# Kernel optimization log

Measured on AMD Instinct MI355X. Metric: run time of the kernel, lower is better.

## Reference

```python
import jax, jax.numpy as jnp
import numpy as np

N_NODES = 20000
N_EDGES = 40000
H = 64          # n_hidden
F_ATOM = 62     # n_atom_features (< H, triggers zero-pad path)
F_BOND = 6      # n_bond_features
B = 512         # number of graphs in batch
T = 2           # message passing steps


def setup_inputs() -> dict:
    key = jax.random.key(0)
    ks = jax.random.split(key, 20)
    s = 0.05  # small init scale to avoid selu/tanh saturation
    inp = {
        'node_features': jax.random.normal(ks[0], (N_NODES, F_ATOM), jnp.float32),
        'edge_features': jax.random.normal(ks[1], (N_EDGES, F_BOND), jnp.float32),
        'edge_domain': jax.random.randint(ks[2], (N_EDGES,), 0, N_NODES, jnp.int32),
        'edge_range': jax.random.randint(ks[3], (N_EDGES,), 0, N_NODES, jnp.int32),
        'graph_id': jnp.sort(jax.random.randint(ks[4], (N_NODES,), 0, B, jnp.int32)),
        # EdgeNetwork params (weights stored [in, out], i.e. torch W.T)
        'Wm': jax.random.normal(ks[5], (F_BOND, H), jnp.float32) * s,
        'bm': jnp.zeros((H,), jnp.float32),
        'Ew': jax.random.normal(ks[6], (H, H * H), jnp.float32) * s,  # E.weight used as mm(mlp, E.weight): [H, H*H]
        # update2 linears (T=2)
        'Wu0': jax.random.normal(ks[7], (H, H), jnp.float32) * s,
        'bu0': jnp.zeros((H,), jnp.float32),
        'Wu1': jax.random.normal(ks[8], (H, H), jnp.float32) * s,
        'bu1': jnp.zeros((H,), jnp.float32),
        # atom_embed
        'Wae': jax.random.normal(ks[9], (H, H), jnp.float32) * s,
        'bae': jnp.zeros((H,), jnp.float32),
        # AggregateReadout.R
        'WR': jax.random.normal(ks[10], (H, H), jnp.float32) * s,
        'bR': jnp.zeros((H,), jnp.float32),
        # mlp + out head
        'Wmlp': jax.random.normal(ks[11], (H, H), jnp.float32) * s,
        'bmlp': jnp.zeros((H,), jnp.float32),
        'Wout': jax.random.normal(ks[12], (H, 1), jnp.float32) * s,
        'bout': jnp.zeros((1,), jnp.float32),
    }
    return inp


def reference(node_features, edge_features, edge_domain, edge_range, graph_id,
              Wm, bm, Ew, Wu0, bu0, Wu1, bu1, Wae, bae, WR, bR,
              Wmlp, bmlp, Wout, bout):
    # pad node features up to n_hidden (original zero-pads when narrower)
    h = jnp.pad(node_features, ((0, 0), (0, H - F_ATOM)))  # [N, H]

    # EdgeNetwork: edge-conditioned per-edge HxH weight matrix.
    # Edge features are constant across T, so A is identical each step;
    # compute once (original recomputes the same values every iteration).
    mlp_features = jax.nn.relu(edge_features @ Wm + bm)      # [E, H]
    A = (mlp_features @ Ew).reshape(-1, H, H)                # [E, H, H]

    for Wu, bu in ((Wu0, bu0), (Wu1, bu1)):
        hj = h[edge_range]                                   # gather [E, H]
        edge_message = jnp.einsum('eij,ej->ei', A, hj)       # bmm [E, H]
        message = jax.ops.segment_sum(edge_message, edge_domain,
                                      num_segments=N_NODES)  # scatter-add [N, H]
        h = jax.nn.selu(message @ Wu + bu + h)

    atom_embedding = h @ Wae + bae                           # [N, H]
    # AggregateReadout
    atom_activation = jax.nn.selu(atom_embedding @ WR + bR)  # [N, H]
    graph_sum = jax.ops.segment_sum(atom_activation, graph_id, num_segments=B)
    graph_embedding = jnp.tanh(graph_sum)                    # [B, H]

    mlp_out = jax.nn.relu(graph_embedding @ Wmlp + bmlp)     # [B, H]
    out = mlp_out @ Wout + bout                              # [B, 1]
    return out.reshape(-1, 1)
```

## Files before the change

kernel.cpp:

```cpp
#include <hip/hip_runtime.h>
#include <math.h>

#define NN 20000
#define NE 40000
#define H 64
#define F_ATOM 62
#define F_BOND 6
#define NB 512

typedef _Float16 f16x8 __attribute__((ext_vector_type(8)));
typedef float f32x16 __attribute__((ext_vector_type(16)));

__device__ __forceinline__ float selu_f(float x) {
    const float scale = 1.0507009873554805f;
    const float alpha = 1.6732632423543772f;
    return scale * (x > 0.0f ? x : alpha * (__expf(x) - 1.0f));
}

__device__ __forceinline__ f16x8 splat8h(_Float16 x) {
    union { _Float16 h[2]; unsigned u; } p;
    p.h[0] = x; p.h[1] = x;
    union { unsigned u[4]; f16x8 v; } r;
    r.u[0] = p.u; r.u[1] = p.u; r.u[2] = p.u; r.u[3] = p.u;
    return r.v;
}

__global__ void prep_kernel(const float* __restrict__ nf, const float* __restrict__ ef,
                            const float* __restrict__ Wm, const float* __restrict__ bm,
                            const float* __restrict__ Ew,
                            _Float16* __restrict__ h_h,
                            unsigned* __restrict__ mlp2, _Float16* __restrict__ ewb,
                            float* __restrict__ msg, float* __restrict__ gsum) {
    const int bid = blockIdx.x;
    const int t = threadIdx.x;
    if (bid < 625) {
        __shared__ float st[64][65];
        const int el = t & 63;
        const int ig = t >> 6;
        const int e = bid * 64 + el;
        const float* efe = ef + e * F_BOND;
        const float e0 = efe[0], e1 = efe[1], e2 = efe[2];
        const float e3 = efe[3], e4 = efe[4], e5 = efe[5];
#pragma unroll
        for (int p = 0; p < 16; ++p) {
            const int i = ig * 16 + p;
            float s = bm[i];
            s = fmaf(e0, Wm[0 * H + i], s);
            s = fmaf(e1, Wm[1 * H + i], s);
            s = fmaf(e2, Wm[2 * H + i], s);
            s = fmaf(e3, Wm[3 * H + i], s);
            s = fmaf(e4, Wm[4 * H + i], s);
            s = fmaf(e5, Wm[5 * H + i], s);
            st[i][el] = fmaxf(s, 0.0f);
        }
        __syncthreads();
        const int p = t >> 3;
        const int ch = t & 7;
#pragma unroll
        for (int j = 0; j < 8; ++j) {
            const int e_l = ch * 8 + j;
            union { unsigned u; _Float16 hh[2]; } pk;
            pk.hh[0] = (_Float16)st[2 * p][e_l];
            pk.hh[1] = (_Float16)st[2 * p + 1][e_l];
            mlp2[(size_t)p * NE + bid * 64 + e_l] = pk.u;
        }
    } else if (bid < 5625) {
        int idx = (bid - 625) * 256 + t;
        int n = idx >> 6, c = idx & 63;
        h_h[idx] = (_Float16)((c < F_ATOM) ? nf[n * F_ATOM + c] : 0.0f);
    } else if (bid < 5753) {
        int tid = (bid - 5625) * 256 + t;
        int l = tid & 63;
        int nt = (tid >> 6) & 1;
        int c = tid >> 7;
        int kk = c >> 2;
        int jbase = (c & 3) * 16 + (l >> 5) * 8;
        int i = nt * 32 + (l & 31);
        const float* src = Ew + kk * 4096 + i * 64 + jbase;
        _Float16* dst = ewb + tid * 8;
#pragma unroll
        for (int u = 0; u < 8; ++u) dst[u] = (_Float16)src[u];
    } else if (bid < 7003) {
        int idx = (bid - 5753) * 256 + t;
        reinterpret_cast<float4*>(msg)[idx] = make_float4(0.f, 0.f, 0.f, 0.f);
    } else {
        int idx = (bid - 7003) * 256 + t;
        reinterpret_cast<float4*>(gsum)[idx] = make_float4(0.f, 0.f, 0.f, 0.f);
    }
}

__global__ __launch_bounds__(128, 4) void edge_message_mfma(
    const _Float16* __restrict__ h_h, const unsigned* __restrict__ mlp2,
    const int* __restrict__ ed, const int* __restrict__ er,
    const _Float16* __restrict__ ewb, float* __restrict__ msg)
{
    __shared__ char sm[32768];
    __shared__ int edom_s[64];

    const int t = threadIdx.x;
    const int lane = t & 63;
    const int kg = t >> 6;
    const int l31 = lane & 31;
    const int hf = lane >> 5;
    const int kh = blockIdx.x & 1;
    const int eb = (blockIdx.x >> 1) * 64;
    const int kbase = kh * 32 + kg * 16;

    if (t < 64) edom_s[t] = ed[eb + t];

    const int eA = eb + l31;
    const int eB = eA + 32;
    const int gA = er[eA], gB = er[eB];

    f16x8 hjA[4], hjB[4];
#pragma unroll
    for (int cq = 0; cq < 4; ++cq) {
        hjA[cq] = *reinterpret_cast<const f16x8*>(h_h + gA * 64 + cq * 16 + hf * 8);
        hjB[cq] = *reinterpret_cast<const f16x8*>(h_h + gB * 64 + cq * 16 + hf * 8);
    }

    unsigned mvA[8], mvB[8];
#pragma unroll
    for (int pp = 0; pp < 8; ++pp) {
        mvA[pp] = mlp2[(size_t)((kbase >> 1) + pp) * NE + eA];
        mvB[pp] = mlp2[(size_t)((kbase >> 1) + pp) * NE + eB];
    }

    asm volatile("s_waitcnt vmcnt(0)" ::: "memory");

    char* wbase = sm + kg * 16384;
    auto stage = [&](int s) {
        const char* gs = reinterpret_cast<const char*>(ewb) +
                         ((size_t)(kbase + s) << 13) + lane * 16;
        char* lb = wbase + (s & 1) * 8192 + lane * 16;
#pragma unroll
        for (int r = 0; r < 8; ++r) {
            __builtin_amdgcn_global_load_lds(
                (const __attribute__((address_space(1))) void*)(gs + r * 1024),
                (__attribute__((address_space(3))) void*)(lb + r * 1024),
                16, 0, 0);
        }
    };

    f32x16 a00, a01, a10, a11;
#pragma unroll
    for (int i = 0; i < 16; ++i) { a00[i] = 0.f; a01[i] = 0.f; a10[i] = 0.f; a11[i] = 0.f; }

    stage(0);

#pragma unroll
    for (int s = 0; s < 16; ++s) {
        asm volatile("s_waitcnt vmcnt(0)" ::: "memory");
        if (s < 15) stage(s + 1);
        const char* buf = wbase + (s & 1) * 8192;
        union { unsigned u; _Float16 hh[2]; } ua, ub;
        ua.u = mvA[s >> 1]; ub.u = mvB[s >> 1];
        f16x8 sA = splat8h(ua.hh[s & 1]);
        f16x8 sB = splat8h(ub.hh[s & 1]);
        __builtin_amdgcn_s_setprio(1);
#pragma unroll
        for (int cq = 0; cq < 4; ++cq) {
            f16x8 b0 = *reinterpret_cast<const f16x8*>(buf + (cq * 2 + 0) * 1024 + lane * 16);
            f16x8 b1 = *reinterpret_cast<const f16x8*>(buf + (cq * 2 + 1) * 1024 + lane * 16);
            f16x8 aA = sA * hjA[cq];
            f16x8 aB = sB * hjB[cq];
            a00 = __builtin_amdgcn_mfma_f32_32x32x16_f16(aA, b0, a00, 0, 0, 0);
            a01 = __builtin_amdgcn_mfma_f32_32x32x16_f16(aA, b1, a01, 0, 0, 0);
            a10 = __builtin_amdgcn_mfma_f32_32x32x16_f16(aB, b0, a10, 0, 0, 0);
            a11 = __builtin_amdgcn_mfma_f32_32x32x16_f16(aB, b1, a11, 0, 0, 0);
        }
        __builtin_amdgcn_s_setprio(0);
    }

    float* X = reinterpret_cast<float*>(sm);
    __syncthreads();
    if (kg == 1) {
#pragma unroll
        for (int r = 0; r < 16; ++r) {
            const int m = (r & 3) + 8 * (r >> 2) + 4 * hf;
            X[m * 64 + l31]             = a00[r];
            X[m * 64 + 32 + l31]        = a01[r];
            X[(32 + m) * 64 + l31]      = a10[r];
            X[(32 + m) * 64 + 32 + l31] = a11[r];
        }
    }
    __syncthreads();
    if (kg == 0) {
#pragma unroll
        for (int r = 0; r < 16; ++r) {
            const int m = (r & 3) + 8 * (r >> 2) + 4 * hf;
            const int domA = edom_s[m];
            const int domB = edom_s[32 + m];
            atomicAdd(&msg[domA * 64 + l31],      a00[r] + X[m * 64 + l31]);
            atomicAdd(&msg[domA * 64 + 32 + l31], a01[r] + X[m * 64 + 32 + l31]);
            atomicAdd(&msg[domB * 64 + l31],      a10[r] + X[(32 + m) * 64 + l31]);
            atomicAdd(&msg[domB * 64 + 32 + l31], a11[r] + X[(32 + m) * 64 + 32 + l31]);
        }
    }
}

__global__ __launch_bounds__(256) void node_update_kernel(
    float* __restrict__ msg, const float* __restrict__ Wu,
    const float* __restrict__ bu, _Float16* __restrict__ h_h) {
    __shared__ float ms[32][65];
    const int t = threadIdx.x;
    const int nb = blockIdx.x * 32;
#pragma unroll
    for (int r = 0; r < 2; ++r) {
        int idx = r * 256 + t;
        int n = idx >> 4, c4 = (idx & 15) * 4;
        float4* src = reinterpret_cast<float4*>(msg + (size_t)(nb + n) * 64 + c4);
        float4 v = *src;
        *src = make_float4(0.f, 0.f, 0.f, 0.f);
        ms[n][c4 + 0] = v.x; ms[n][c4 + 1] = v.y;
        ms[n][c4 + 2] = v.z; ms[n][c4 + 3] = v.w;
    }
    __syncthreads();
    const int i = t & 63;
    const int n0 = (t >> 6) * 8;
    float acc[8];
#pragma unroll
    for (int j = 0; j < 8; ++j) acc[j] = bu[i];
#pragma unroll 8
    for (int k = 0; k < 64; ++k) {
        float w = Wu[k * 64 + i];
#pragma unroll
        for (int j = 0; j < 8; ++j) acc[j] = fmaf(ms[n0 + j][k], w, acc[j]);
    }
#pragma unroll
    for (int j = 0; j < 8; ++j) {
        int o = (nb + n0 + j) * 64 + i;
        h_h[o] = (_Float16)selu_f(acc[j] + (float)h_h[o]);
    }
}

__global__ __launch_bounds__(256) void upd2_embed_readout(
    const float* __restrict__ msg, const float* __restrict__ Wu,
    const float* __restrict__ bu, const _Float16* __restrict__ h_h,
    const float* __restrict__ Wae, const float* __restrict__ bae,
    const float* __restrict__ WR, const float* __restrict__ bR,
    const int* __restrict__ gid, float* __restrict__ gsum) {
    __shared__ float ms[32][65];
    __shared__ float hn[32][65];
    __shared__ float ae[32][65];
    const int t = threadIdx.x;
    const int nb = blockIdx.x * 32;
#pragma unroll
    for (int r = 0; r < 2; ++r) {
        int idx = r * 256 + t;
        int n = idx >> 4, c4 = (idx & 15) * 4;
        float4 v = *reinterpret_cast<const float4*>(msg + (size_t)(nb + n) * 64 + c4);
        ms[n][c4 + 0] = v.x; ms[n][c4 + 1] = v.y;
        ms[n][c4 + 2] = v.z; ms[n][c4 + 3] = v.w;
    }
    __syncthreads();
    const int i = t & 63;
    const int n0 = (t >> 6) * 8;
    float acc[8];
#pragma unroll
    for (int j = 0; j < 8; ++j) acc[j] = bu[i];
#pragma unroll 8
    for (int k = 0; k < 64; ++k) {
        float w = Wu[k * 64 + i];
#pragma unroll
        for (int j = 0; j < 8; ++j) acc[j] = fmaf(ms[n0 + j][k], w, acc[j]);
    }
#pragma unroll
    for (int j = 0; j < 8; ++j)
        hn[n0 + j][i] = selu_f(acc[j] + (float)h_h[(nb + n0 + j) * 64 + i]);
    __syncthreads();
#pragma unroll
    for (int j = 0; j < 8; ++j) acc[j] = bae[i];
#pragma unroll 8
    for (int k = 0; k < 64; ++k) {
        float w = Wae[k * 64 + i];
#pragma unroll
        for (int j = 0; j < 8; ++j) acc[j] = fmaf(hn[n0 + j][k], w, acc[j]);
    }
#pragma unroll
    for (int j = 0; j < 8; ++j) ae[n0 + j][i] = acc[j];
    __syncthreads();
#pragma unroll
    for (int j = 0; j < 8; ++j) acc[j] = bR[i];
#pragma unroll 8
    for (int k = 0; k < 64; ++k) {
        float w = WR[k * 64 + i];
#pragma unroll
        for (int j = 0; j < 8; ++j) acc[j] = fmaf(ae[n0 + j][k], w, acc[j]);
    }
#pragma unroll
    for (int j = 0; j < 8; ++j)
        atomicAdd(&gsum[gid[nb + n0 + j] * 64 + i], selu_f(acc[j]));
}

__global__ void final_kernel(const float* __restrict__ gsum, const float* __restrict__ Wmlp,
                             const float* __restrict__ bmlp, const float* __restrict__ Wout,
                             const float* __restrict__ bout, float* __restrict__ out) {
    __shared__ float ge[64];
    int g = blockIdx.x, i = threadIdx.x;
    ge[i] = tanhf(gsum[g * H + i]);
    __syncthreads();
    float s = bmlp[i];
#pragma unroll
    for (int k = 0; k < H; ++k) s = fmaf(ge[k], Wmlp[k * H + i], s);
    float mo = fmaxf(s, 0.0f) * Wout[i];
#pragma unroll
    for (int off = 32; off > 0; off >>= 1) mo += __shfl_down(mo, off);
    if (i == 0) out[g] = mo + bout[0];
}

extern "C" void kernel_launch(void* const* d_in, const int* in_sizes, int n_in,
                              void* d_out, int out_size, void* d_ws, size_t ws_size,
                              hipStream_t stream) {
    const float* nf   = (const float*)d_in[0];
    const float* ef   = (const float*)d_in[1];
    const int*   ed   = (const int*)d_in[2];
    const int*   er   = (const int*)d_in[3];
    const int*   gid  = (const int*)d_in[4];
    const float* Wm   = (const float*)d_in[5];
    const float* bm   = (const float*)d_in[6];
    const float* Ew   = (const float*)d_in[7];
    const float* Wu0  = (const float*)d_in[8];
    const float* bu0  = (const float*)d_in[9];
    const float* Wu1  = (const float*)d_in[10];
    const float* bu1  = (const float*)d_in[11];
    const float* Wae  = (const float*)d_in[12];
    const float* bae  = (const float*)d_in[13];
    const float* WR   = (const float*)d_in[14];
    const float* bR   = (const float*)d_in[15];
    const float* Wmlp = (const float*)d_in[16];
    const float* bmlp = (const float*)d_in[17];
    const float* Wout = (const float*)d_in[18];
    const float* bout = (const float*)d_in[19];
    float* out = (float*)d_out;

    float* ws = (float*)d_ws;
    float*    msg  = ws + 1280000;
    float*    gsum = ws + 2560000;
    unsigned* mlp2 = (unsigned*)(ws + 2592768);
    _Float16* h_h  = (_Float16*)(ws + 3872768);
    _Float16* ewb  = (_Float16*)(ws + 4512768);

    prep_kernel<<<7035, 256, 0, stream>>>(nf, ef, Wm, bm, Ew, h_h, mlp2, ewb, msg, gsum);

    edge_message_mfma<<<1250, 128, 0, stream>>>(h_h, mlp2, ed, er, ewb, msg);
    node_update_kernel<<<NN / 32, 256, 0, stream>>>(msg, Wu0, bu0, h_h);
    edge_message_mfma<<<1250, 128, 0, stream>>>(h_h, mlp2, ed, er, ewb, msg);
    upd2_embed_readout<<<NN / 32, 256, 0, stream>>>(msg, Wu1, bu1, h_h,
                                                    Wae, bae, WR, bR, gid, gsum);

    final_kernel<<<NB, 64, 0, stream>>>(gsum, Wmlp, bmlp, Wout, bout, out);
}
```

Before: 137.9 us.

## Keep Ew slices register-resident and stream edge tiles through persistent blocks

The edge message kernel is restructured so that each wave loads a fixed slice of the fp16 Ew weights into registers once. It then loops over five 32-edge tiles, using the weights as the MFMA A operand and the scaled gathered node features as B. This replaces the per-block streaming of weights through LDS with double buffering. Partial sums across the k-split waves are reduced in LDS with shared atomics before global atomics go to msg. The cost is 128 registers of weights per lane, fewer blocks (500 blocks of 512 threads), extra barriers per tile, and LDS atomic contention.

```diff
diff --git a/kernel.cpp b/kernel.cpp
--- a/kernel.cpp
+++ b/kernel.cpp
@@ -29,7 +29,7 @@
                             const float* __restrict__ Wm, const float* __restrict__ bm,
                             const float* __restrict__ Ew,
                             _Float16* __restrict__ h_h,
-                            unsigned* __restrict__ mlp2, _Float16* __restrict__ ewb,
+                            unsigned* __restrict__ mlp2, _Float16* __restrict__ ewA,
                             float* __restrict__ msg, float* __restrict__ gsum) {
     const int bid = blockIdx.x;
     const int t = threadIdx.x;
@@ -70,14 +70,18 @@
         h_h[idx] = (_Float16)((c < F_ATOM) ? nf[n * F_ATOM + c] : 0.0f);
     } else if (bid < 5753) {
         int tid = (bid - 5625) * 256 + t;
-        int l = tid & 63;
-        int nt = (tid >> 6) & 1;
-        int c = tid >> 7;
-        int kk = c >> 2;
-        int jbase = (c & 3) * 16 + (l >> 5) * 8;
-        int i = nt * 32 + (l & 31);
-        const float* src = Ew + kk * 4096 + i * 64 + jbase;
-        _Float16* dst = ewb + tid * 8;
+        const int l = tid & 63;
+        const int f = (tid >> 6) & 31;
+        const int slice = tid >> 11;
+        const int kh = slice >> 3;
+        const int kw = (slice >> 1) & 3;
+        const int ih = slice & 1;
+        const int i = ih * 32 + (l & 31);
+        const int kg = kh * 2048 + kw * 512 + f * 16 + (l >> 5) * 8;
+        const int kk = kg >> 6;
+        const int jb = kg & 63;
+        const float* src = Ew + (size_t)kk * 4096 + i * 64 + jb;
+        _Float16* dst = ewA + (size_t)tid * 8;
 #pragma unroll
         for (int u = 0; u < 8; ++u) dst[u] = (_Float16)src[u];
     } else if (bid < 7003) {
@@ -89,113 +93,85 @@
     }
 }
 
-__global__ __launch_bounds__(128, 4) void edge_message_mfma(
+__global__ __launch_bounds__(512, 1) void edge_message_mfma(
     const _Float16* __restrict__ h_h, const unsigned* __restrict__ mlp2,
     const int* __restrict__ ed, const int* __restrict__ er,
-    const _Float16* __restrict__ ewb, float* __restrict__ msg)
+    const _Float16* __restrict__ ewA, float* __restrict__ msg)
 {
-    __shared__ char sm[32768];
-    __shared__ int edom_s[64];
+    __shared__ float sm[2 * 32 * 33];
+    __shared__ int edom_t[32];
 
     const int t = threadIdx.x;
     const int lane = t & 63;
-    const int kg = t >> 6;
+    const int w = t >> 6;
     const int l31 = lane & 31;
     const int hf = lane >> 5;
+    const int ih = w & 1;
+    const int kw = w >> 1;
     const int kh = blockIdx.x & 1;
-    const int eb = (blockIdx.x >> 1) * 64;
-    const int kbase = kh * 32 + kg * 16;
-
-    if (t < 64) edom_s[t] = ed[eb + t];
-
-    const int eA = eb + l31;
-    const int eB = eA + 32;
-    const int gA = er[eA], gB = er[eB];
-
-    f16x8 hjA[4], hjB[4];
-#pragma unroll
-    for (int cq = 0; cq < 4; ++cq) {
-        hjA[cq] = *reinterpret_cast<const f16x8*>(h_h + gA * 64 + cq * 16 + hf * 8);
-        hjB[cq] = *reinterpret_cast<const f16x8*>(h_h + gB * 64 + cq * 16 + hf * 8);
-    }
-
-    unsigned mvA[8], mvB[8];
-#pragma unroll
-    for (int pp = 0; pp < 8; ++pp) {
-        mvA[pp] = mlp2[(size_t)((kbase >> 1) + pp) * NE + eA];
-        mvB[pp] = mlp2[(size_t)((kbase >> 1) + pp) * NE + eB];
-    }
-
-    asm volatile("s_waitcnt vmcnt(0)" ::: "memory");
-
-    char* wbase = sm + kg * 16384;
-    auto stage = [&](int s) {
-        const char* gs = reinterpret_cast<const char*>(ewb) +
-                         ((size_t)(kbase + s) << 13) + lane * 16;
-        char* lb = wbase + (s & 1) * 8192 + lane * 16;
-#pragma unroll
-        for (int r = 0; r < 8; ++r) {
-            __builtin_amdgcn_global_load_lds(
-                (const __attribute__((address_space(1))) void*)(gs + r * 1024),
-                (__attribute__((address_space(3))) void*)(lb + r * 1024),
-                16, 0, 0);
-        }
-    };
-
-    f32x16 a00, a01, a10, a11;
-#pragma unroll
-    for (int i = 0; i < 16; ++i) { a00[i] = 0.f; a01[i] = 0.f; a10[i] = 0.f; a11[i] = 0.f; }
-
-    stage(0);
-
-#pragma unroll
-    for (int s = 0; s < 16; ++s) {
-        asm volatile("s_waitcnt vmcnt(0)" ::: "memory");
-        if (s < 15) stage(s + 1);
-        const char* buf = wbase + (s & 1) * 8192;
-        union { unsigned u; _Float16 hh[2]; } ua, ub;
-        ua.u = mvA[s >> 1]; ub.u = mvB[s >> 1];
-        f16x8 sA = splat8h(ua.hh[s & 1]);
-        f16x8 sB = splat8h(ub.hh[s & 1]);
+    const int group = blockIdx.x >> 1;
+    const int ebase0 = group * 160;
+
+    const int slice = kh * 8 + kw * 2 + ih;
+    f16x8 A[32];
+    {
+        const _Float16* ap = ewA + (size_t)slice * 16384 + lane * 8;
+#pragma unroll
+        for (int f = 0; f < 32; ++f)
+            A[f] = *reinterpret_cast<const f16x8*>(ap + f * 512);
+    }
+
+    for (int idx = t; idx < 2 * 32 * 33; idx += 512) sm[idx] = 0.0f;
+    __syncthreads();
+
+    const int kkbase = kh * 32 + kw * 8;
+
+    for (int tile = 0; tile < 5; ++tile) {
+        const int eb = ebase0 + tile * 32;
+        if (w == 0 && lane < 32) edom_t[lane] = ed[eb + lane];
+
+        const int e = eb + l31;
+        const int g0 = er[e];
+        f16x8 hj[4];
+#pragma unroll
+        for (int cq = 0; cq < 4; ++cq)
+            hj[cq] = *reinterpret_cast<const f16x8*>(h_h + g0 * 64 + cq * 16 + hf * 8);
+        unsigned mv[4];
+#pragma unroll
+        for (int pp = 0; pp < 4; ++pp)
+            mv[pp] = mlp2[(size_t)((kkbase >> 1) + pp) * NE + e];
+
+        f32x16 acc;
+#pragma unroll
+        for (int i = 0; i < 16; ++i) acc[i] = 0.f;
+
         __builtin_amdgcn_s_setprio(1);
 #pragma unroll
-        for (int cq = 0; cq < 4; ++cq) {
-            f16x8 b0 = *reinterpret_cast<const f16x8*>(buf + (cq * 2 + 0) * 1024 + lane * 16);
-            f16x8 b1 = *reinterpret_cast<const f16x8*>(buf + (cq * 2 + 1) * 1024 + lane * 16);
-            f16x8 aA = sA * hjA[cq];
-            f16x8 aB = sB * hjB[cq];
-            a00 = __builtin_amdgcn_mfma_f32_32x32x16_f16(aA, b0, a00, 0, 0, 0);
-            a01 = __builtin_amdgcn_mfma_f32_32x32x16_f16(aA, b1, a01, 0, 0, 0);
-            a10 = __builtin_amdgcn_mfma_f32_32x32x16_f16(aB, b0, a10, 0, 0, 0);
-            a11 = __builtin_amdgcn_mfma_f32_32x32x16_f16(aB, b1, a11, 0, 0, 0);
+        for (int f = 0; f < 32; ++f) {
+            union { unsigned u; _Float16 hh[2]; } ua;
+            ua.u = mv[f >> 3];
+            f16x8 b = splat8h(ua.hh[(f >> 2) & 1]) * hj[f & 3];
+            acc = __builtin_amdgcn_mfma_f32_32x32x16_f16(A[f], b, acc, 0, 0, 0);
         }
         __builtin_amdgcn_s_setprio(0);
-    }
-
-    float* X = reinterpret_cast<float*>(sm);
-    __syncthreads();
-    if (kg == 1) {
+
 #pragma unroll
         for (int r = 0; r < 16; ++r) {
             const int m = (r & 3) + 8 * (r >> 2) + 4 * hf;
-            X[m * 64 + l31]             = a00[r];
-            X[m * 64 + 32 + l31]        = a01[r];
-            X[(32 + m) * 64 + l31]      = a10[r];
-            X[(32 + m) * 64 + 32 + l31] = a11[r];
-        }
-    }
-    __syncthreads();
-    if (kg == 0) {
-#pragma unroll
-        for (int r = 0; r < 16; ++r) {
-            const int m = (r & 3) + 8 * (r >> 2) + 4 * hf;
-            const int domA = edom_s[m];
-            const int domB = edom_s[32 + m];
-            atomicAdd(&msg[domA * 64 + l31],      a00[r] + X[m * 64 + l31]);
-            atomicAdd(&msg[domA * 64 + 32 + l31], a01[r] + X[m * 64 + 32 + l31]);
-            atomicAdd(&msg[domB * 64 + l31],      a10[r] + X[(32 + m) * 64 + l31]);
-            atomicAdd(&msg[domB * 64 + 32 + l31], a11[r] + X[(32 + m) * 64 + 32 + l31]);
-        }
+            atomicAdd(&sm[ih * 1056 + m * 33 + l31], acc[r]);
+        }
+        __syncthreads();
+
+#pragma unroll
+        for (int q = 0; q < 4; ++q) {
+            const int el = w * 4 + q;
+            const int dom = edom_t[el];
+            const float v = sm[(lane >> 5) * 1056 + (lane & 31) * 33 + el];
+            atomicAdd(&msg[(size_t)dom * 64 + lane], v);
+        }
+        __syncthreads();
+        for (int idx = t; idx < 2 * 32 * 33; idx += 512) sm[idx] = 0.0f;
+        __syncthreads();
     }
 }
 
@@ -339,13 +315,13 @@
     float*    gsum = ws + 2560000;
     unsigned* mlp2 = (unsigned*)(ws + 2592768);
     _Float16* h_h  = (_Float16*)(ws + 3872768);
-    _Float16* ewb  = (_Float16*)(ws + 4512768);
-
-    prep_kernel<<<7035, 256, 0, stream>>>(nf, ef, Wm, bm, Ew, h_h, mlp2, ewb, msg, gsum);
-
-    edge_message_mfma<<<1250, 128, 0, stream>>>(h_h, mlp2, ed, er, ewb, msg);
+    _Float16* ewA  = (_Float16*)(ws + 4512768);
+
+    prep_kernel<<<7035, 256, 0, stream>>>(nf, ef, Wm, bm, Ew, h_h, mlp2, ewA, msg, gsum);
+
+    edge_message_mfma<<<500, 512, 0, stream>>>(h_h, mlp2, ed, er, ewA, msg);
     node_update_kernel<<<NN / 32, 256, 0, stream>>>(msg, Wu0, bu0, h_h);
-    edge_message_mfma<<<1250, 128, 0, stream>>>(h_h, mlp2, ed, er, ewb, msg);
+    edge_message_mfma<<<500, 512, 0, stream>>>(h_h, mlp2, ed, er, ewA, msg);
     upd2_embed_readout<<<NN / 32, 256, 0, stream>>>(msg, Wu1, bu1, h_h,
                                                     Wae, bae, WR, bR, gid, gsum);
 
```

Result: slower. 306.7 us (+122.4%).
